# Optimization experiments

Measured on AMD Instinct MI355X. Metric: run time of the kernel, lower is better.

The kernel has to match this reference:

```python
import jax, jax.numpy as jnp
import numpy as np
import math

B, T, D, H = 2, 2048, 2048, 16
HD = D // H  # head_dim = 128


def setup_inputs() -> dict:
    key = jax.random.key(0)
    ks = jax.random.split(key, 9)
    s = 1.0 / math.sqrt(D)
    return {
        "x": jax.random.normal(ks[0], (B, T, D), dtype=jnp.float32),
        "Wq": jax.random.normal(ks[1], (D, D), dtype=jnp.float32) * s,
        "bq": jax.random.normal(ks[2], (D,), dtype=jnp.float32) * 0.01,
        "Wk": jax.random.normal(ks[3], (D, D), dtype=jnp.float32) * s,
        "bk": jax.random.normal(ks[4], (D,), dtype=jnp.float32) * 0.01,
        "Wv": jax.random.normal(ks[5], (D, D), dtype=jnp.float32) * s,
        "bv": jax.random.normal(ks[6], (D,), dtype=jnp.float32) * 0.01,
        "Wo": jax.random.normal(ks[7], (D, D), dtype=jnp.float32) * s,
        "bo": jax.random.normal(ks[8], (D,), dtype=jnp.float32) * 0.01,
    }


def reference(x, Wq, bq, Wk, bk, Wv, bv, Wo, bo):
    b, t, c = x.shape
    # projections; split heads: (B,T,D) -> (B,H,T,HD)
    def split_heads(y):
        return y.reshape(b, t, H, HD).transpose(0, 2, 1, 3)

    q = split_heads(x @ Wq + bq)
    k = split_heads(x @ Wk + bk)
    v = split_heads(x @ Wv + bv)

    scale = 1.0 / math.sqrt(HD)
    attn = jnp.einsum('bhqd,bhkd->bhqk', q, k) * scale  # (B,H,T,T)
    # causal mask (prefill path: past_k is None)
    causal = jnp.tril(jnp.ones((t, t), dtype=bool))
    attn = jnp.where(causal, attn, -jnp.inf)
    attn = jax.nn.softmax(attn, axis=-1)
    out = jnp.einsum('bhqk,bhkd->bhqd', attn, v)  # (B,H,T,HD)
    out = out.transpose(0, 2, 1, 3).reshape(b, t, c)
    out = out @ Wo + bo
    return (out, k, v)
```

## Files before the change

### kernel.cpp

```cpp
#include <hip/hip_runtime.h>
#include <hip/hip_bf16.h>

#define B_ 2
#define T_ 2048
#define D_ 2048
#define H_ 16
#define HD_ 128
#define M_ 4096

typedef __attribute__((ext_vector_type(8))) short short8;
typedef __attribute__((ext_vector_type(8))) __bf16 bf16x8;
typedef __attribute__((ext_vector_type(4))) float f32x4;
typedef __attribute__((ext_vector_type(4))) unsigned uint32x4;

__device__ __forceinline__ short f2bf(float f) {
  unsigned u = __builtin_bit_cast(unsigned, f);
  u += 0x7fffu + ((u >> 16) & 1u);
  return (short)(u >> 16);
}

__device__ __forceinline__ unsigned cvtpk(float lo, float hi) {
  unsigned r;
  asm("v_cvt_pk_bf16_f32 %0, %1, %2" : "=v"(r) : "v"(lo), "v"(hi));
  return r;
}

__device__ __forceinline__ float ex2(float x) {
  float r;
  asm("v_exp_f32 %0, %1" : "=v"(r) : "v"(x));
  return r;
}

__device__ __forceinline__ void gl_lds16(const void* g, void* l) {
  __builtin_amdgcn_global_load_lds(
      (const __attribute__((address_space(1))) unsigned int*)g,
      (__attribute__((address_space(3))) unsigned int*)l, 16, 0, 0);
}

__device__ __forceinline__ f32x4 mfma_bf16(short8 a, short8 b, f32x4 c) {
  return __builtin_amdgcn_mfma_f32_16x16x32_bf16(
      __builtin_bit_cast(bf16x8, a), __builtin_bit_cast(bf16x8, b), c, 0, 0, 0);
}

__device__ __forceinline__ float2 sw16f(float x) {
  float a = x, bv;
  asm("v_mov_b32 %0, %1" : "=v"(bv) : "v"(x));
  asm("v_permlane16_swap_b32 %0, %1" : "+v"(a), "+v"(bv));
  return make_float2(a, bv);
}
__device__ __forceinline__ float2 sw32f(float x) {
  float a = x, bv;
  asm("v_mov_b32 %0, %1" : "=v"(bv) : "v"(x));
  asm("v_permlane32_swap_b32 %0, %1" : "+v"(a), "+v"(bv));
  return make_float2(a, bv);
}
__device__ __forceinline__ void sw16u(unsigned x, unsigned& e, unsigned& o) {
  unsigned a = x, bv;
  asm("v_mov_b32 %0, %1" : "=v"(bv) : "v"(x));
  asm("v_permlane16_swap_b32 %0, %1" : "+v"(a), "+v"(bv));
  e = a; o = bv;
}
__device__ __forceinline__ void pl32u(unsigned& a, unsigned& b) {
  asm("v_permlane32_swap_b32 %0, %1" : "+v"(a), "+v"(b));
}

__global__ void cast_f32_bf16(const float* __restrict__ in, short* __restrict__ out, int n4) {
  int i = blockIdx.x * blockDim.x + threadIdx.x;
  int stride = gridDim.x * blockDim.x;
  for (; i < n4; i += stride) {
    float4 v = ((const float4*)in)[i];
    short4 s;
    s.x = f2bf(v.x); s.y = f2bf(v.y); s.z = f2bf(v.z); s.w = f2bf(v.w);
    ((short4*)out)[i] = s;
  }
}

__global__ void transpose_cast_w4(const float* __restrict__ Wq, const float* __restrict__ Wk,
                                  const float* __restrict__ Wv, const float* __restrict__ Wo,
                                  short* __restrict__ wqkv, short* __restrict__ wo) {
  __shared__ float t[32][33];
  int z = blockIdx.z;
  const float* W = z == 0 ? Wq : z == 1 ? Wk : z == 2 ? Wv : Wo;
  short* dst = z < 3 ? wqkv + (size_t)z * D_ * D_ : wo;
  int n0 = blockIdx.x * 32, k0 = blockIdx.y * 32;
  int tx = threadIdx.x, ty = threadIdx.y;
#pragma unroll
  for (int j = 0; j < 4; ++j)
    t[ty + j * 8][tx] = W[(size_t)(k0 + ty + j * 8) * D_ + n0 + tx];
  __syncthreads();
#pragma unroll
  for (int j = 0; j < 4; ++j)
    dst[(size_t)(n0 + ty + j * 8) * D_ + k0 + tx] = f2bf(t[tx][ty + j * 8]);
}

__global__ __launch_bounds__(512, 2) void gemm_qkv(
    const short* __restrict__ A, const short* __restrict__ Bt,
    const float* __restrict__ b0, const float* __restrict__ b1,
    const float* __restrict__ b2,
    short* __restrict__ q_o, short* __restrict__ k_o,
    float* __restrict__ kf_o, float* __restrict__ vf_o,
    short* __restrict__ vt_o) {
  __shared__ __attribute__((aligned(16))) char lds[2][57344];
  const int K = D_, NT = K / 64;

  int d = blockIdx.x;
  int lg = (d & 7) * 64 + (d >> 3);
  int m0 = (lg & 15) * 256, n0 = (lg >> 4) * 192;

  int tid = threadIdx.x, lane = tid & 63, wid = tid >> 6;
  int wm = wid >> 2, wn = wid & 3;
  int lr = lane & 15, g = lane >> 4;

  int rowA = tid >> 2;
  int cA = ((((tid & 3) << 4) ^ (((rowA >> 1) & 3) << 4)) >> 1);
  const short* aS = A + (size_t)(m0 + rowA) * K + cA;
  int rowB = tid >> 3;
  int cB = ((((tid & 7) << 4) ^ ((rowB & 7) << 4)) >> 1);
  const short* bS = Bt + (size_t)(n0 + rowB) * K + cB;
  char* ldsb = (char*)lds;

  auto stageA = [&](int ts, int kh) {
    char* dst = ldsb + (ts & 1) * 57344 + kh * 16384 + tid * 16;
    const short* s = aS + ts * 64 + kh * 32;
    gl_lds16(s, dst);
    gl_lds16(s + (size_t)128 * K, dst + 8192);
  };
  auto stageB = [&](int ts) {
    char* dst = ldsb + (ts & 1) * 57344 + 32768 + tid * 16;
    const short* s = bS + ts * 64;
    gl_lds16(s, dst);
    gl_lds16(s + (size_t)64 * K, dst + 8192);
    gl_lds16(s + (size_t)128 * K, dst + 16384);
  };

  int swzA = (g * 16) ^ (((lr >> 1) & 3) << 4);
  int aoff = (wm * 128 + lr) * 64 + swzA;
  int boff0 = (wn * 48 + lr) * 128 + ((g * 16) ^ ((lr & 7) << 4));
  int boff1 = (wn * 48 + lr) * 128 + ((64 + g * 16) ^ ((lr & 7) << 4));

  f32x4 acc[8][3] = {};

  stageA(0, 0); stageB(0); stageA(0, 1); stageA(1, 0);
  asm volatile("s_waitcnt vmcnt(4)" ::: "memory");
  __builtin_amdgcn_s_barrier();
  __builtin_amdgcn_sched_barrier(0);

#pragma unroll 1
  for (int t = 0; t < NT; ++t) {
    const char* base = ldsb + (t & 1) * 57344;
    int t1 = (t + 1 < NT) ? t + 1 : NT - 1;
    int t2 = (t + 2 < NT) ? t + 2 : NT - 1;
    short8 afr[8], bfr[3];

#pragma unroll
    for (int mi = 0; mi < 8; ++mi) afr[mi] = *(const short8*)(base + aoff + mi * 1024);
#pragma unroll
    for (int ni = 0; ni < 3; ++ni) bfr[ni] = *(const short8*)(base + 32768 + boff0 + ni * 2048);
    stageA(t1, 1); stageB(t1);
    __builtin_amdgcn_s_setprio(1);
#pragma unroll
    for (int mi = 0; mi < 8; ++mi)
#pragma unroll
      for (int ni = 0; ni < 3; ++ni)
        acc[mi][ni] = mfma_bf16(afr[mi], bfr[ni], acc[mi][ni]);
    __builtin_amdgcn_s_setprio(0);
    asm volatile("s_waitcnt vmcnt(7)" ::: "memory");
    __builtin_amdgcn_s_barrier();
    __builtin_amdgcn_sched_barrier(0);

#pragma unroll
    for (int mi = 0; mi < 8; ++mi) afr[mi] = *(const short8*)(base + 16384 + aoff + mi * 1024);
#pragma unroll
    for (int ni = 0; ni < 3; ++ni) bfr[ni] = *(const short8*)(base + 32768 + boff1 + ni * 2048);
    stageA(t2, 0);
    __builtin_amdgcn_s_setprio(1);
#pragma unroll
    for (int mi = 0; mi < 8; ++mi)
#pragma unroll
      for (int ni = 0; ni < 3; ++ni)
        acc[mi][ni] = mfma_bf16(afr[mi], bfr[ni], acc[mi][ni]);
    __builtin_amdgcn_s_setprio(0);
    asm volatile("s_waitcnt vmcnt(2)" ::: "memory");
    __builtin_amdgcn_s_barrier();
    __builtin_amdgcn_sched_barrier(0);
  }

#pragma unroll
  for (int ni = 0; ni < 3; ++ni) {
    int gcb = n0 + wn * 48 + ni * 16;
    int region = gcb >> 11;
    int nc = (gcb & 2047) + lr;
    int hh = nc >> 7, hd = nc & 127;
    const float* bias = region == 0 ? b0 : region == 1 ? b1 : b2;
    float bv = bias[nc];
#pragma unroll
    for (int mi = 0; mi < 8; ++mi) {
      int gr0 = m0 + wm * 128 + mi * 16 + (g << 2);
      int bb = gr0 >> 11, tt0 = gr0 & 2047;
      size_t hbase = (size_t)(bb * H_ + hh);
      float v0 = acc[mi][ni][0] + bv;
      float v1 = acc[mi][ni][1] + bv;
      float v2 = acc[mi][ni][2] + bv;
      float v3 = acc[mi][ni][3] + bv;
      size_t ib = (hbase * T_ + tt0) * HD_ + hd;
      if (region == 0) {
        q_o[ib] = f2bf(v0); q_o[ib + HD_] = f2bf(v1);
        q_o[ib + 2 * HD_] = f2bf(v2); q_o[ib + 3 * HD_] = f2bf(v3);
      } else if (region == 1) {
        k_o[ib] = f2bf(v0); k_o[ib + HD_] = f2bf(v1);
        k_o[ib + 2 * HD_] = f2bf(v2); k_o[ib + 3 * HD_] = f2bf(v3);
        kf_o[ib] = v0; kf_o[ib + HD_] = v1;
        kf_o[ib + 2 * HD_] = v2; kf_o[ib + 3 * HD_] = v3;
      } else {
        vf_o[ib] = v0; vf_o[ib + HD_] = v1;
        vf_o[ib + 2 * HD_] = v2; vf_o[ib + 3 * HD_] = v3;
        short4 s4;
        s4.x = f2bf(v0); s4.y = f2bf(v1); s4.z = f2bf(v2); s4.w = f2bf(v3);
        *(short4*)&vt_o[(hbase * HD_ + hd) * T_ + tt0] = s4;
      }
    }
  }
}

__global__ __launch_bounds__(256, 2) void gemm_rb(
    const short* __restrict__ A, const short* __restrict__ Bt,
    const float* __restrict__ b0, float* __restrict__ f_o) {
  __shared__ __attribute__((aligned(16))) short lds[4][2][4096];
  const int K = D_, NT = K / 32;

  int nx = gridDim.x, nwg = nx * gridDim.y;
  int d = blockIdx.y * nx + blockIdx.x;
  int cpx = nwg >> 3;
  int lg = (d & 7) * cpx + (d >> 3);
  int m0 = (lg / nx) * 128, n0 = (lg % nx) * 128;

  int tid = threadIdx.x, lane = tid & 63, w = tid >> 6;
  int wm = w >> 1, wn = w & 1;
  int lr = lane & 15, g = lane >> 4;

  int o1 = tid * 16, o2 = 4096 + tid * 16;
  int row1 = tid >> 2, row2 = 64 + row1;
  int cb = (tid & 3) << 4;
  int c1 = (cb ^ (((row1 >> 1) & 3) << 4)) >> 1;
  int c2 = (cb ^ (((row2 >> 1) & 3) << 4)) >> 1;
  const short* aS1 = A + (size_t)(m0 + row1) * K + c1;
  const short* aS2 = A + (size_t)(m0 + row2) * K + c2;
  const short* bS1 = Bt + (size_t)(n0 + row1) * K + c1;
  const short* bS2 = Bt + (size_t)(n0 + row2) * K + c2;

  int aoff[4], boff[4];
#pragma unroll
  for (int i = 0; i < 4; ++i) {
    int ra = wm * 64 + i * 16 + lr;
    aoff[i] = ra * 64 + ((g * 16) ^ (((ra >> 1) & 3) << 4));
    int rb = wn * 64 + i * 16 + lr;
    boff[i] = rb * 64 + ((g * 16) ^ (((rb >> 1) & 3) << 4));
  }

  f32x4 acc[4][4] = {};

#pragma unroll
  for (int s = 0; s < 3; ++s) {
    char* la = (char*)&lds[s][0][0];
    char* lb = (char*)&lds[s][1][0];
    gl_lds16(aS1 + s * 32, la + o1);
    gl_lds16(aS2 + s * 32, la + o2);
    gl_lds16(bS1 + s * 32, lb + o1);
    gl_lds16(bS2 + s * 32, lb + o2);
  }
  asm volatile("s_waitcnt vmcnt(8)" ::: "memory");
  __builtin_amdgcn_s_barrier();
  __builtin_amdgcn_sched_barrier(0);

#pragma unroll 1
  for (int t4 = 0; t4 < NT; t4 += 4) {
#pragma unroll
    for (int p = 0; p < 4; ++p) {
      int t = t4 + p;
      {
        int ts = (t + 3 < NT) ? t + 3 : NT - 1;
        char* la = (char*)&lds[(p + 3) & 3][0][0];
        char* lb = (char*)&lds[(p + 3) & 3][1][0];
        gl_lds16(aS1 + ts * 32, la + o1);
        gl_lds16(aS2 + ts * 32, la + o2);
        gl_lds16(bS1 + ts * 32, lb + o1);
        gl_lds16(bS2 + ts * 32, lb + o2);
      }
      const char* la = (const char*)&lds[p][0][0];
      const char* lb = (const char*)&lds[p][1][0];
      short8 af[4], bfv[4];
#pragma unroll
      for (int i = 0; i < 4; ++i) {
        af[i] = *(const short8*)(la + aoff[i]);
        bfv[i] = *(const short8*)(lb + boff[i]);
      }
      __builtin_amdgcn_s_setprio(1);
#pragma unroll
      for (int mi = 0; mi < 4; ++mi)
#pragma unroll
        for (int ni = 0; ni < 4; ++ni)
          acc[mi][ni] = mfma_bf16(af[mi], bfv[ni], acc[mi][ni]);
      __builtin_amdgcn_s_setprio(0);
      asm volatile("s_waitcnt vmcnt(8)" ::: "memory");
      __builtin_amdgcn_s_barrier();
      __builtin_amdgcn_sched_barrier(0);
    }
  }

#pragma unroll
  for (int mi = 0; mi < 4; ++mi) {
#pragma unroll
    for (int ni = 0; ni < 4; ++ni) {
      int gr0 = m0 + wm * 64 + mi * 16 + (g << 2);
      int gc = n0 + wn * 64 + ni * 16 + lr;
      float bv = b0[gc];
#pragma unroll
      for (int r = 0; r < 4; ++r)
        f_o[(size_t)(gr0 + r) * D_ + gc] = acc[mi][ni][r] + bv;
    }
  }
}

__global__ __launch_bounds__(256, 2) void attn_fwd(
    const short* __restrict__ qb, const short* __restrict__ kb,
    const short* __restrict__ vtb, short* __restrict__ aob) {
  __shared__ __attribute__((aligned(16))) char kvlds[2][16384];

  int d = blockIdx.x;
  int bh = d & 31;
  int qt = 31 - (d >> 5);
  int tid = threadIdx.x, w = tid >> 6, lane = tid & 63;
  int lr = lane & 15, g = lane >> 4;
  const short* Q  = qb  + (size_t)bh * T_ * HD_;
  const short* Kp = kb  + (size_t)bh * T_ * HD_;
  const short* Vt = vtb + (size_t)bh * HD_ * T_;
  const float scale2 = 0.12751879202f;
  int b = bh >> 4, h = bh & 15;
  bool hi16 = (lane & 16) != 0;

  int oA = ((2 * w + 0) * 64 + lane) * 16;
  int oB = ((2 * w + 1) * 64 + lane) * 16;
  int rKA = oA >> 8, rKB = oB >> 8;
  size_t skA = (size_t)rKA * HD_ + (((oA & 255) ^ ((rKA & 7) << 4)) >> 1);
  size_t skB = (size_t)rKB * HD_ + (((oB & 255) ^ ((rKB & 7) << 4)) >> 1);
  int rVA = oA >> 6, rVB = oB >> 6;
  size_t svA = (size_t)rVA * T_ + (((oA & 63) ^ (((rVA >> 1) & 3) << 4)) >> 1);
  size_t svB = (size_t)rVB * T_ + (((oB & 63) ^ (((rVB >> 1) & 3) << 4)) >> 1);

  int q0 = qt * 64 + w * 16;
  int ntiles = 2 * qt + 2;

  {
    char* kd = &kvlds[0][0];
    char* vd = &kvlds[0][8192];
    gl_lds16(Kp + skA, kd + oA);
    gl_lds16(Kp + skB, kd + oB);
    gl_lds16(Vt + svA, vd + oA);
    gl_lds16(Vt + svB, vd + oB);
  }

  short8 qf[4];
#pragma unroll
  for (int kk = 0; kk < 4; ++kk)
    qf[kk] = *(const short8*)&Q[(size_t)(q0 + lr) * HD_ + kk * 32 + g * 8];

  f32x4 o[8] = {};
  float mrow = -1e30f, lrow = 0.f;
  __syncthreads();

#pragma unroll 1
  for (int t = 0; t < ntiles; ++t) {
    int kv0 = t * 32, buf = t & 1;
    if (t + 1 < ntiles) {
      char* kd = &kvlds[buf ^ 1][0];
      char* vd = &kvlds[buf ^ 1][8192];
      const short* Kn = Kp + (size_t)(kv0 + 32) * HD_;
      const short* Vn = Vt + (kv0 + 32);
      gl_lds16(Kn + skA, kd + oA);
      gl_lds16(Kn + skB, kd + oB);
      gl_lds16(Vn + svA, vd + oA);
      gl_lds16(Vn + svB, vd + oB);
    }
    if (kv0 < q0 + 16) {
      const char* kb_ = &kvlds[buf][0];
      const char* vb_ = &kvlds[buf][8192];
      short8 kf0[4], kf1[4], vf[8];
#pragma unroll
      for (int kk = 0; kk < 4; ++kk) {
        int cs = (kk * 64 + g * 16) ^ ((lr & 7) << 4);
        kf0[kk] = *(const short8*)(kb_ + (lr * 256 + cs));
        kf1[kk] = *(const short8*)(kb_ + ((16 + lr) * 256 + cs));
      }
#pragma unroll
      for (int f = 0; f < 8; ++f)
        vf[f] = *(const short8*)(vb_ + ((f * 16 + lr) * 64 +
                 ((g * 16) ^ (((lr >> 1) & 3) << 4))));

      f32x4 s0 = {}, s1 = {};
      __builtin_amdgcn_s_setprio(1);
#pragma unroll
      for (int kk = 0; kk < 4; ++kk) {
        s0 = mfma_bf16(kf0[kk], qf[kk], s0);
        s1 = mfma_bf16(kf1[kk], qf[kk], s1);
      }
      __builtin_amdgcn_s_setprio(0);

      float vv[8];
#pragma unroll
      for (int r = 0; r < 4; ++r) {
        vv[r] = s0[r] * scale2;
        vv[4 + r] = s1[r] * scale2;
      }
      if (kv0 + 31 > q0) {
        int qrow = q0 + lr;
#pragma unroll
        for (int r = 0; r < 4; ++r) {
          if (kv0 + 4 * g + r > qrow) vv[r] = -1e30f;
          if (kv0 + 16 + 4 * g + r > qrow) vv[4 + r] = -1e30f;
        }
      }

      float pm = vv[0];
#pragma unroll
      for (int i = 1; i < 8; ++i) pm = fmaxf(pm, vv[i]);
      { float2 tpm = sw32f(pm); pm = fmaxf(tpm.x, tpm.y); }
      { float2 tpm = sw16f(pm); pm = fmaxf(tpm.x, tpm.y); }

      bool rescale = !__all(pm - mrow <= 11.54f);
      float alpha = 1.0f;
      if (rescale) {
        float mnew = fmaxf(mrow, pm);
        alpha = ex2(mrow - mnew);
        mrow = mnew;
      }

      float p[8];
      float rs = 0.f;
#pragma unroll
      for (int i = 0; i < 8; ++i) { p[i] = ex2(vv[i] - mrow); rs += p[i]; }
      { float2 trs = sw32f(rs); rs = trs.x + trs.y; }
      { float2 trs = sw16f(rs); rs = trs.x + trs.y; }
      lrow = (rescale ? lrow * alpha : lrow) + rs;

      if (rescale) {
        float alr[4];
#pragma unroll
        for (int r = 0; r < 4; ++r) alr[r] = __shfl(alpha, 4 * g + r);
#pragma unroll
        for (int f = 0; f < 8; ++f)
#pragma unroll
          for (int r = 0; r < 4; ++r) o[f][r] *= alr[r];
      }

      unsigned w0 = cvtpk(p[0], p[1]), w1 = cvtpk(p[2], p[3]);
      unsigned w2 = cvtpk(p[4], p[5]), w3 = cvtpk(p[6], p[7]);
      unsigned e0, od0, e1, od1, e2, od2, e3, od3;
      sw16u(w0, e0, od0); sw16u(w1, e1, od1);
      sw16u(w2, e2, od2); sw16u(w3, e3, od3);
      unsigned F0 = e0,  S0 = e2;  pl32u(F0, S0);
      unsigned F1 = e1,  S1 = e3;  pl32u(F1, S1);
      unsigned F2 = od0, S2 = od2; pl32u(F2, S2);
      unsigned F3 = od1, S3 = od3; pl32u(F3, S3);
      uint32x4 paw = { hi16 ? S0 : F0, hi16 ? S1 : F1,
                       hi16 ? S2 : F2, hi16 ? S3 : F3 };
      short8 pa = __builtin_bit_cast(short8, paw);

      __builtin_amdgcn_s_setprio(1);
#pragma unroll
      for (int f = 0; f < 8; ++f) o[f] = mfma_bf16(pa, vf[f], o[f]);
      __builtin_amdgcn_s_setprio(0);
    }
    __syncthreads();
  }

  float inv = 1.0f / lrow;
  float invr[4];
#pragma unroll
  for (int r = 0; r < 4; ++r) invr[r] = __shfl(inv, 4 * g + r);
#pragma unroll
  for (int r = 0; r < 4; ++r) {
    int q = q0 + 4 * g + r;
    size_t rowoff = ((size_t)(b * T_ + q)) * D_ + h * HD_;
#pragma unroll
    for (int f = 0; f < 8; ++f)
      aob[rowoff + f * 16 + lr] = f2bf(o[f][r] * invr[r]);
  }
}

extern "C" void kernel_launch(void* const* d_in, const int* in_sizes, int n_in,
                              void* d_out, int out_size, void* d_ws, size_t ws_size,
                              hipStream_t stream) {
  const float* x  = (const float*)d_in[0];
  const float* Wq = (const float*)d_in[1];
  const float* bq = (const float*)d_in[2];
  const float* Wk = (const float*)d_in[3];
  const float* bk = (const float*)d_in[4];
  const float* Wv = (const float*)d_in[5];
  const float* bv = (const float*)d_in[6];
  const float* Wo = (const float*)d_in[7];
  const float* bo = (const float*)d_in[8];
  float* out  = (float*)d_out;
  float* kout = out + (size_t)M_ * D_;
  float* vout = kout + (size_t)M_ * D_;

  char* ws = (char*)d_ws;
  auto alloc = [&](size_t bytes) {
    char* p = ws;
    ws += (bytes + 255) & ~(size_t)255;
    return p;
  };
  short* xb    = (short*)alloc((size_t)M_ * D_ * 2);
  short* wqkvT = (short*)alloc((size_t)3 * D_ * D_ * 2);
  short* woT   = (short*)alloc((size_t)D_ * D_ * 2);
  short* qb    = (short*)alloc((size_t)M_ * D_ * 2);
  short* kb    = (short*)alloc((size_t)M_ * D_ * 2);
  short* vtb   = (short*)alloc((size_t)M_ * D_ * 2);
  short* aob = xb;

  cast_f32_bf16<<<2048, 256, 0, stream>>>(x, xb, M_ * D_ / 4);
  dim3 tb(32, 8);
  transpose_cast_w4<<<dim3(64, 64, 4), tb, 0, stream>>>(Wq, Wk, Wv, Wo, wqkvT, woT);

  gemm_qkv<<<512, 512, 0, stream>>>(xb, wqkvT, bq, bk, bv, qb, kb, kout, vout, vtb);
  attn_fwd<<<1024, 256, 0, stream>>>(qb, kb, vtb, aob);
  gemm_rb<<<dim3(16, 32), 256, 0, stream>>>(aob, woT, bo, out);
}
```

Measured before the change: 246.7 us.

## Load QKV GEMM B fragments directly into registers instead of staging via LDS

The B (weight) tile of the fused QKV GEMM is no longer staged through shared memory; each wave loads its own B fragments straight from global memory into double-buffered registers, prefetching the next k-tile. This halves the LDS footprint per block and removes LDS writes and reads for B, but B data is no longer shared across the waves in a row (each of the two wm waves reloads it). The loop is unrolled by two to ping-pong the register buffers, and the vmcnt waits are retuned to the new count of outstanding loads. The risks are more global/L2 traffic, higher register pressure and less coalesced direct loads.

```diff
diff --git a/kernel.cpp b/kernel.cpp
--- a/kernel.cpp
+++ b/kernel.cpp
@@ -100,7 +100,7 @@
     short* __restrict__ q_o, short* __restrict__ k_o,
     float* __restrict__ kf_o, float* __restrict__ vf_o,
     short* __restrict__ vt_o) {
-  __shared__ __attribute__((aligned(16))) char lds[2][57344];
+  __shared__ __attribute__((aligned(16))) char lds[2][2][16384];
   const int K = D_, NT = K / 64;
 
   int d = blockIdx.x;
@@ -114,75 +114,81 @@
   int rowA = tid >> 2;
   int cA = ((((tid & 3) << 4) ^ (((rowA >> 1) & 3) << 4)) >> 1);
   const short* aS = A + (size_t)(m0 + rowA) * K + cA;
-  int rowB = tid >> 3;
-  int cB = ((((tid & 7) << 4) ^ ((rowB & 7) << 4)) >> 1);
-  const short* bS = Bt + (size_t)(n0 + rowB) * K + cB;
-  char* ldsb = (char*)lds;
 
   auto stageA = [&](int ts, int kh) {
-    char* dst = ldsb + (ts & 1) * 57344 + kh * 16384 + tid * 16;
+    char* dst = &lds[ts & 1][kh][0] + tid * 16;
     const short* s = aS + ts * 64 + kh * 32;
     gl_lds16(s, dst);
     gl_lds16(s + (size_t)128 * K, dst + 8192);
   };
-  auto stageB = [&](int ts) {
-    char* dst = ldsb + (ts & 1) * 57344 + 32768 + tid * 16;
-    const short* s = bS + ts * 64;
-    gl_lds16(s, dst);
-    gl_lds16(s + (size_t)64 * K, dst + 8192);
-    gl_lds16(s + (size_t)128 * K, dst + 16384);
+
+  const short* bb0 = Bt + (size_t)(n0 + wn * 48 + lr) * K + g * 8;
+  const short* bb1 = bb0 + (size_t)16 * K;
+  const short* bb2 = bb0 + (size_t)32 * K;
+
+  short8 B0[3][2], B1[3][2];
+  auto loadB = [&](int ts, short8 (&Bn)[3][2]) {
+    int off = ts * 64;
+#pragma unroll
+    for (int kh = 0; kh < 2; ++kh) {
+      Bn[0][kh] = *(const short8*)(bb0 + off + kh * 32);
+      Bn[1][kh] = *(const short8*)(bb1 + off + kh * 32);
+      Bn[2][kh] = *(const short8*)(bb2 + off + kh * 32);
+    }
   };
 
   int swzA = (g * 16) ^ (((lr >> 1) & 3) << 4);
   int aoff = (wm * 128 + lr) * 64 + swzA;
-  int boff0 = (wn * 48 + lr) * 128 + ((g * 16) ^ ((lr & 7) << 4));
-  int boff1 = (wn * 48 + lr) * 128 + ((64 + g * 16) ^ ((lr & 7) << 4));
 
   f32x4 acc[8][3] = {};
 
-  stageA(0, 0); stageB(0); stageA(0, 1); stageA(1, 0);
-  asm volatile("s_waitcnt vmcnt(4)" ::: "memory");
+  stageA(0, 0); stageA(0, 1); stageA(1, 0);
+  loadB(0, B0);
+  asm volatile("s_waitcnt vmcnt(6)" ::: "memory");
   __builtin_amdgcn_s_barrier();
   __builtin_amdgcn_sched_barrier(0);
 
-#pragma unroll 1
-  for (int t = 0; t < NT; ++t) {
-    const char* base = ldsb + (t & 1) * 57344;
+  auto TILE = [&](int t, short8 (&Bc)[3][2], short8 (&Bn)[3][2]) {
+    const char* base0 = &lds[t & 1][0][0];
+    const char* base1 = &lds[t & 1][1][0];
     int t1 = (t + 1 < NT) ? t + 1 : NT - 1;
     int t2 = (t + 2 < NT) ? t + 2 : NT - 1;
-    short8 afr[8], bfr[3];
-
-#pragma unroll
-    for (int mi = 0; mi < 8; ++mi) afr[mi] = *(const short8*)(base + aoff + mi * 1024);
-#pragma unroll
-    for (int ni = 0; ni < 3; ++ni) bfr[ni] = *(const short8*)(base + 32768 + boff0 + ni * 2048);
-    stageA(t1, 1); stageB(t1);
+    short8 afr[8];
+
+#pragma unroll
+    for (int mi = 0; mi < 8; ++mi) afr[mi] = *(const short8*)(base0 + aoff + mi * 1024);
+    stageA(t1, 1);
+    loadB(t1, Bn);
     __builtin_amdgcn_s_setprio(1);
 #pragma unroll
     for (int mi = 0; mi < 8; ++mi)
 #pragma unroll
       for (int ni = 0; ni < 3; ++ni)
-        acc[mi][ni] = mfma_bf16(afr[mi], bfr[ni], acc[mi][ni]);
+        acc[mi][ni] = mfma_bf16(afr[mi], Bc[ni][0], acc[mi][ni]);
     __builtin_amdgcn_s_setprio(0);
-    asm volatile("s_waitcnt vmcnt(7)" ::: "memory");
+    asm volatile("s_waitcnt vmcnt(10)" ::: "memory");
     __builtin_amdgcn_s_barrier();
     __builtin_amdgcn_sched_barrier(0);
 
 #pragma unroll
-    for (int mi = 0; mi < 8; ++mi) afr[mi] = *(const short8*)(base + 16384 + aoff + mi * 1024);
-#pragma unroll
-    for (int ni = 0; ni < 3; ++ni) bfr[ni] = *(const short8*)(base + 32768 + boff1 + ni * 2048);
+    for (int mi = 0; mi < 8; ++mi) afr[mi] = *(const short8*)(base1 + aoff + mi * 1024);
     stageA(t2, 0);
     __builtin_amdgcn_s_setprio(1);
 #pragma unroll
     for (int mi = 0; mi < 8; ++mi)
 #pragma unroll
       for (int ni = 0; ni < 3; ++ni)
-        acc[mi][ni] = mfma_bf16(afr[mi], bfr[ni], acc[mi][ni]);
+        acc[mi][ni] = mfma_bf16(afr[mi], Bc[ni][1], acc[mi][ni]);
     __builtin_amdgcn_s_setprio(0);
-    asm volatile("s_waitcnt vmcnt(2)" ::: "memory");
+    asm volatile("s_waitcnt vmcnt(10)" ::: "memory");
     __builtin_amdgcn_s_barrier();
     __builtin_amdgcn_sched_barrier(0);
+  };
+
+#pragma unroll 1
+  for (int t = 0; t < NT; t += 2) {
+    TILE(t, B0, B1);
+    TILE(t + 1, B1, B0);
   }
 
 #pragma unroll
```

Result: slower. 300.2 us (+21.7%).
